# Optimization experiments

Hardware: AMD Instinct MI355X
Metric: run time of the kernel (lower is better)

The kernel has to match this reference:

```python
import jax, jax.numpy as jnp
import numpy as np

ALG = 8  # octonion algebra dimension
_TRIPLES = [(1,2,3),(1,4,5),(1,7,6),(2,4,6),(2,5,7),(3,4,7),(3,6,5)]

def _oct_table():
    # Cayley multiplication table: e_i * e_j = S[i,j] * e_{K[i,j]}
    K = np.zeros((8,8), np.int64); S = np.zeros((8,8), np.int64)
    K[0,:] = np.arange(8); S[0,:] = 1
    K[:,0] = np.arange(8); S[:,0] = 1
    for i in range(1,8):
        K[i,i] = 0; S[i,i] = -1
    for (a,b,c) in _TRIPLES:
        for x,y,z in ((a,b,c),(b,c,a),(c,a,b)):
            K[x,y] = z; S[x,y] = 1
            K[y,x] = z; S[y,x] = -1
    return K, S

_K, _S = _oct_table()

def _ternary(w):
    # BitNet-style absmean ternary quantization (STE is irrelevant for fwd)
    scale = jnp.mean(jnp.abs(w)) + 1e-8
    wq = jnp.clip(jnp.round(w / scale), -1.0, 1.0) * scale
    return w + jax.lax.stop_gradient(wq - w)

def _oct_big(w):
    # w: [8, din8, dout8] -> structured dense [8*din8, 8*dout8]
    # out_k = sum_{i,j: e_i e_j = s e_k} s * x_i @ W_j  (64 static blocks)
    din8, dout8 = w.shape[1], w.shape[2]
    big = jnp.zeros((8, din8, 8, dout8), w.dtype)
    for i in range(8):
        for j in range(8):
            big = big.at[i, :, int(_K[i, j]), :].set(float(_S[i, j]) * w[j])
    return big.reshape(8 * din8, 8 * dout8)

def _oct_linear(x, w):
    return x @ _oct_big(_ternary(w))

def setup_inputs() -> dict:
    key = jax.random.key(0)
    k1, k2, k3, k4 = jax.random.split(key, 4)
    B, T, D = 8, 4096, 768
    H = 2048  # int(2*4*768/3) rounded up to multiple of 8
    d8, h8 = D // ALG, H // ALG
    x = jax.random.normal(k1, (B, T, D), dtype=jnp.float32)
    w_gate = 0.02 * jax.random.normal(k2, (ALG, d8, h8), dtype=jnp.float32)
    w_up   = 0.02 * jax.random.normal(k3, (ALG, d8, h8), dtype=jnp.float32)
    w_down = 0.02 * jax.random.normal(k4, (ALG, h8, d8), dtype=jnp.float32)
    return {"x": x, "w_gate": w_gate, "w_up": w_up, "w_down": w_down}

def reference(x, w_gate, w_up, w_down):
    gate = _oct_linear(x, w_gate)          # [B,T,H]
    up   = _oct_linear(x, w_up)            # [B,T,H]
    h    = jax.nn.silu(gate) * up          # SwiGLU gate
    return _oct_linear(h, w_down)          # [B,T,D]
```

## Files before the change

### kernel.cpp

```cpp
#include <hip/hip_runtime.h>
#include <hip/hip_bf16.h>

typedef unsigned short u16;
typedef unsigned int u32;
typedef float f32x4 __attribute__((ext_vector_type(4)));
typedef __bf16 bf16x8 __attribute__((ext_vector_type(8)));

#define AS1 __attribute__((address_space(1)))
#define AS3 __attribute__((address_space(3)))

#define MTOT 32768
#define DK   768
#define HN   2048

__constant__ signed char J_TAB[64] = {
  0,1,2,3,4,5,6,7,
  1,0,3,2,5,4,7,6,
  2,3,0,1,6,7,4,5,
  3,2,1,0,7,6,5,4,
  4,5,6,7,0,1,2,3,
  5,4,7,6,1,0,3,2,
  6,7,4,5,2,3,0,1,
  7,6,5,4,3,2,1,0};
__constant__ signed char S_TAB[64] = {
   1, 1, 1, 1, 1, 1, 1, 1,
  -1, 1,-1, 1,-1, 1, 1,-1,
  -1, 1, 1,-1,-1,-1, 1, 1,
  -1,-1, 1, 1,-1, 1,-1, 1,
  -1, 1, 1, 1, 1,-1,-1,-1,
  -1,-1, 1,-1, 1, 1, 1,-1,
  -1,-1,-1, 1, 1,-1, 1, 1,
  -1, 1,-1,-1, 1, 1,-1, 1};

__device__ __forceinline__ u16 f2bf(float f) {
  u32 x = __float_as_uint(f);
  x += 0x7fffu + ((x >> 16) & 1u);
  return (u16)(x >> 16);
}

__device__ __forceinline__ void gload_lds16(const void* g, void* l) {
  __builtin_amdgcn_global_load_lds((AS1 void*)(g), (AS3 void*)(l), 16, 0, 0);
}

template <int ROWS>
__device__ __forceinline__ void stage_tile(const u16* __restrict__ src, int ldk,
                                           u16* lds, int tid) {
#pragma unroll
  for (int f0 = 0; f0 < ROWS * 8; f0 += 256) {
    int flat = f0 + tid;
    int row = flat >> 3;
    int c = (flat & 7) ^ (row & 7);
    gload_lds16(src + row * ldk + c * 8, lds + (f0 + (tid & 192)) * 8);
  }
}

__device__ __forceinline__ bf16x8 frag64(const u16* lds, int row, int cbase) {
  int c = cbase ^ (row & 7);
  return *(const bf16x8*)(lds + row * 64 + c * 8);
}

__global__ void scales1_kernel(const float* __restrict__ w0,
                               const float* __restrict__ w1,
                               const float* __restrict__ w2,
                               float* __restrict__ partials) {
  __shared__ float red[256];
  const int t = blockIdx.x / 192;
  const int chunk = blockIdx.x % 192;
  const float* w = (t == 0) ? w0 : (t == 1) ? w1 : w2;
  const float4* w4 = (const float4*)(w + chunk * 1024);
  float4 v = w4[threadIdx.x];
  red[threadIdx.x] = fabsf(v.x) + fabsf(v.y) + fabsf(v.z) + fabsf(v.w);
  __syncthreads();
  for (int off = 128; off; off >>= 1) {
    if (threadIdx.x < off) red[threadIdx.x] += red[threadIdx.x + off];
    __syncthreads();
  }
  if (threadIdx.x == 0) partials[blockIdx.x] = red[0];
}

__global__ void scales2_kernel(const float* __restrict__ partials,
                               float* __restrict__ scales) {
  __shared__ float red[256];
  float s = (threadIdx.x < 192) ? partials[blockIdx.x * 192 + threadIdx.x] : 0.f;
  red[threadIdx.x] = s;
  __syncthreads();
  for (int off = 128; off; off >>= 1) {
    if (threadIdx.x < off) red[threadIdx.x] += red[threadIdx.x + off];
    __syncthreads();
  }
  if (threadIdx.x == 0) scales[blockIdx.x] = red[0] / 196608.f + 1e-8f;
}

__global__ void build_big_kernel(const float* __restrict__ w,
                                 const float* __restrict__ scales, int sidx,
                                 int A, int B, u16* __restrict__ dst) {
  int idx = blockIdx.x * 256 + threadIdx.x;
  int K8 = 8 * A;
  int n = idx / K8;
  int k = idx - n * K8;
  int i = k / A, a = k - i * A;
  int c = n / B, b = n - c * B;
  float scale = scales[sidx];
  int j = J_TAB[i * 8 + c];
  float q = rintf(w[(j * A + a) * B + b] / scale);
  q = fminf(1.f, fmaxf(-1.f, q));
  dst[idx] = f2bf(q * (float)S_TAB[i * 8 + c]);
}

__global__ void cvt_x_kernel(const float* __restrict__ x, u16* __restrict__ xb) {
  int gid = blockIdx.x * 256 + threadIdx.x;
  const float4* x4 = (const float4*)x;
  float4 v0 = x4[gid * 2], v1 = x4[gid * 2 + 1];
  uint4 o;
  o.x = (u32)f2bf(v0.x) | ((u32)f2bf(v0.y) << 16);
  o.y = (u32)f2bf(v0.z) | ((u32)f2bf(v0.w) << 16);
  o.z = (u32)f2bf(v1.x) | ((u32)f2bf(v1.y) << 16);
  o.w = (u32)f2bf(v1.z) | ((u32)f2bf(v1.w) << 16);
  ((uint4*)xb)[gid] = o;
}

__global__ __launch_bounds__(256) void gemm1_kernel(
    const u16* __restrict__ xb, const u16* __restrict__ wg,
    const u16* __restrict__ wu, const float* __restrict__ scales,
    u16* __restrict__ h) {
  __shared__ __align__(16) u16 lA[128 * 64];
  __shared__ __align__(16) u16 lG[64 * 64];
  __shared__ __align__(16) u16 lU[64 * 64];
  const int tid = threadIdx.x;
  const int bn = blockIdx.x & 31;
  const int bm = blockIdx.x >> 5;
  const int m0 = bm * 128, n0 = bn * 64;
  const int lane = tid & 63, wave = tid >> 6;
  const int wm = wave >> 1, wn = wave & 1;
  const int l15 = lane & 15, quad = lane >> 4;

  f32x4 accG[4][2] = {};
  f32x4 accU[4][2] = {};

  const u16* aSrc = xb + m0 * DK;
  const u16* gSrc = wg + n0 * DK;
  const u16* uSrc = wu + n0 * DK;

  for (int k0 = 0; k0 < DK; k0 += 64) {
    stage_tile<128>(aSrc + k0, DK, lA, tid);
    stage_tile<64>(gSrc + k0, DK, lG, tid);
    stage_tile<64>(uSrc + k0, DK, lU, tid);
    __syncthreads();
#pragma unroll
    for (int ks = 0; ks < 2; ++ks) {
      const int cb = ks * 4 + quad;
      bf16x8 af[4], gf[2], uf[2];
#pragma unroll
      for (int mi = 0; mi < 4; ++mi)
        af[mi] = frag64(lA, wm * 64 + mi * 16 + l15, cb);
#pragma unroll
      for (int ni = 0; ni < 2; ++ni) {
        gf[ni] = frag64(lG, wn * 32 + ni * 16 + l15, cb);
        uf[ni] = frag64(lU, wn * 32 + ni * 16 + l15, cb);
      }
#pragma unroll
      for (int mi = 0; mi < 4; ++mi)
#pragma unroll
        for (int ni = 0; ni < 2; ++ni) {
          accG[mi][ni] = __builtin_amdgcn_mfma_f32_16x16x32_bf16(
              af[mi], gf[ni], accG[mi][ni], 0, 0, 0);
          accU[mi][ni] = __builtin_amdgcn_mfma_f32_16x16x32_bf16(
              af[mi], uf[ni], accU[mi][ni], 0, 0, 0);
        }
    }
    __syncthreads();
  }

  const float sg = scales[0], su = scales[1];
#pragma unroll
  for (int mi = 0; mi < 4; ++mi)
#pragma unroll
    for (int ni = 0; ni < 2; ++ni)
#pragma unroll
      for (int r = 0; r < 4; ++r) {
        int m = m0 + wm * 64 + mi * 16 + quad * 4 + r;
        int n = n0 + wn * 32 + ni * 16 + l15;
        float g = accG[mi][ni][r] * sg;
        float u = accU[mi][ni][r] * su;
        float hv = g / (1.f + __expf(-g)) * u;
        h[m * HN + n] = f2bf(hv);
      }
}

__global__ __launch_bounds__(256) void gemm2_kernel(
    const u16* __restrict__ h, const u16* __restrict__ wd,
    const float* __restrict__ scales, float* __restrict__ out) {
  __shared__ __align__(16) u16 lA[128 * 64];
  __shared__ __align__(16) u16 lB[128 * 64];
  const int tid = threadIdx.x;
  const int bn = blockIdx.x % 6;
  const int bm = blockIdx.x / 6;
  const int m0 = bm * 128, n0 = bn * 128;
  const int lane = tid & 63, wave = tid >> 6;
  const int wm = wave >> 1, wn = wave & 1;
  const int l15 = lane & 15, quad = lane >> 4;

  f32x4 acc[4][4] = {};

  const u16* aSrc = h + m0 * HN;
  const u16* bSrc = wd + n0 * HN;

  for (int k0 = 0; k0 < HN; k0 += 64) {
    stage_tile<128>(aSrc + k0, HN, lA, tid);
    stage_tile<128>(bSrc + k0, HN, lB, tid);
    __syncthreads();
#pragma unroll
    for (int ks = 0; ks < 2; ++ks) {
      const int cb = ks * 4 + quad;
      bf16x8 af[4], bf[4];
#pragma unroll
      for (int mi = 0; mi < 4; ++mi)
        af[mi] = frag64(lA, wm * 64 + mi * 16 + l15, cb);
#pragma unroll
      for (int ni = 0; ni < 4; ++ni)
        bf[ni] = frag64(lB, wn * 64 + ni * 16 + l15, cb);
#pragma unroll
      for (int mi = 0; mi < 4; ++mi)
#pragma unroll
        for (int ni = 0; ni < 4; ++ni)
          acc[mi][ni] = __builtin_amdgcn_mfma_f32_16x16x32_bf16(
              af[mi], bf[ni], acc[mi][ni], 0, 0, 0);
    }
    __syncthreads();
  }

  const float sd = scales[2];
#pragma unroll
  for (int mi = 0; mi < 4; ++mi)
#pragma unroll
    for (int ni = 0; ni < 4; ++ni)
#pragma unroll
      for (int r = 0; r < 4; ++r) {
        int m = m0 + wm * 64 + mi * 16 + quad * 4 + r;
        int n = n0 + wn * 64 + ni * 16 + l15;
        out[m * DK + n] = acc[mi][ni][r] * sd;
      }
}

extern "C" void kernel_launch(void* const* d_in, const int* in_sizes, int n_in,
                              void* d_out, int out_size, void* d_ws, size_t ws_size,
                              hipStream_t stream) {
  const float* x      = (const float*)d_in[0];
  const float* w_gate = (const float*)d_in[1];
  const float* w_up   = (const float*)d_in[2];
  const float* w_down = (const float*)d_in[3];
  float* out = (float*)d_out;

  char* ws = (char*)d_ws;
  float* scales   = (float*)ws;
  float* partials = (float*)(ws + 256);
  u16* wg = (u16*)(ws + 4096);
  u16* wu = (u16*)(ws + 4096 + 1u * 3145728u);
  u16* wd = (u16*)(ws + 4096 + 2u * 3145728u);
  u16* xb = (u16*)(ws + 4096 + 3u * 3145728u);
  u16* h  = (u16*)(ws + 4096 + 3u * 3145728u + 50331648u);

  scales1_kernel<<<576, 256, 0, stream>>>(w_gate, w_up, w_down, partials);
  scales2_kernel<<<3, 256, 0, stream>>>(partials, scales);
  build_big_kernel<<<6144, 256, 0, stream>>>(w_gate, scales, 0, 96, 256, wg);
  build_big_kernel<<<6144, 256, 0, stream>>>(w_up,   scales, 1, 96, 256, wu);
  build_big_kernel<<<6144, 256, 0, stream>>>(w_down, scales, 2, 256, 96, wd);
  cvt_x_kernel<<<12288, 256, 0, stream>>>(x, xb);
  gemm1_kernel<<<8192, 256, 0, stream>>>(xb, wg, wu, scales, h);
  gemm2_kernel<<<1536, 256, 0, stream>>>(h, wd, scales, out);
}
```

Baseline: 597.1 us.

## Pre-swizzle weights into MFMA fragment layout and load B operands directly from global

The weight-building kernel now writes the ternary weight matrices in an MFMA-fragment-ordered layout (16 rows by 32 k per 64-lane line), so each lane can fetch its B fragment with one 16-byte global load. Both GEMMs drop the LDS staging for weights and read B fragments straight from global/L2, which cuts LDS traffic and shared-memory use. gemm1 also widens its N tile from 64 to 128, doubling accumulators and halving the grid. The trade-off is more global-load latency exposed inside the k-loop with no prefetching, plus higher register pressure in gemm1.

```diff
diff --git a/kernel.cpp b/kernel.cpp
--- a/kernel.cpp
+++ b/kernel.cpp
@@ -93,18 +93,28 @@
 
 __global__ void build_big_kernel(const float* __restrict__ w,
                                  const float* __restrict__ scales, int sidx,
-                                 int A, int B, u16* __restrict__ dst) {
-  int idx = blockIdx.x * 256 + threadIdx.x;
-  int K8 = 8 * A;
-  int n = idx / K8;
-  int k = idx - n * K8;
-  int i = k / A, a = k - i * A;
+                                 int A, int B, int KT, u16* __restrict__ dst) {
+  int L = blockIdx.x * 256 + threadIdx.x;
+  int lane = L & 63;
+  int ntkt = L >> 6;
+  int kt = ntkt % KT;
+  int nt = ntkt / KT;
+  int n = nt * 16 + (lane & 15);
+  int kb = kt * 32 + (lane >> 4) * 8;
   int c = n / B, b = n - c * B;
+  int i = kb / A, a0 = kb - i * A;
   float scale = scales[sidx];
+  float s = (float)S_TAB[i * 8 + c];
   int j = J_TAB[i * 8 + c];
-  float q = rintf(w[(j * A + a) * B + b] / scale);
-  q = fminf(1.f, fmaxf(-1.f, q));
-  dst[idx] = f2bf(q * (float)S_TAB[i * 8 + c]);
+  const float* src = w + (j * A + a0) * B + b;
+  u16 vals[8];
+#pragma unroll
+  for (int jj = 0; jj < 8; ++jj) {
+    float q = rintf(src[jj * B] / scale);
+    q = fminf(1.f, fmaxf(-1.f, q));
+    vals[jj] = f2bf(q * s);
+  }
+  *(uint4*)(dst + L * 8) = *(uint4*)vals;
 }
 
 __global__ void cvt_x_kernel(const float* __restrict__ x, u16* __restrict__ xb) {
@@ -120,48 +130,50 @@
 }
 
 __global__ __launch_bounds__(256) void gemm1_kernel(
-    const u16* __restrict__ xb, const u16* __restrict__ wg,
-    const u16* __restrict__ wu, const float* __restrict__ scales,
+    const u16* __restrict__ xb, const u16* __restrict__ wgf,
+    const u16* __restrict__ wuf, const float* __restrict__ scales,
     u16* __restrict__ h) {
   __shared__ __align__(16) u16 lA[128 * 64];
-  __shared__ __align__(16) u16 lG[64 * 64];
-  __shared__ __align__(16) u16 lU[64 * 64];
   const int tid = threadIdx.x;
-  const int bn = blockIdx.x & 31;
-  const int bm = blockIdx.x >> 5;
-  const int m0 = bm * 128, n0 = bn * 64;
+  const int bn = blockIdx.x & 15;
+  const int bm = blockIdx.x >> 4;
+  const int m0 = bm * 128, n0 = bn * 128;
   const int lane = tid & 63, wave = tid >> 6;
   const int wm = wave >> 1, wn = wave & 1;
   const int l15 = lane & 15, quad = lane >> 4;
-
-  f32x4 accG[4][2] = {};
-  f32x4 accU[4][2] = {};
+  const int KT1 = DK / 32;
+
+  f32x4 accG[4][4] = {};
+  f32x4 accU[4][4] = {};
 
   const u16* aSrc = xb + m0 * DK;
-  const u16* gSrc = wg + n0 * DK;
-  const u16* uSrc = wu + n0 * DK;
+  const bf16x8* gLines = (const bf16x8*)wgf;
+  const bf16x8* uLines = (const bf16x8*)wuf;
+  const int ntBase = (n0 + wn * 64) >> 4;
 
   for (int k0 = 0; k0 < DK; k0 += 64) {
     stage_tile<128>(aSrc + k0, DK, lA, tid);
-    stage_tile<64>(gSrc + k0, DK, lG, tid);
-    stage_tile<64>(uSrc + k0, DK, lU, tid);
-    __syncthreads();
+    __syncthreads();
+    const int ktBase = k0 >> 5;
 #pragma unroll
     for (int ks = 0; ks < 2; ++ks) {
+      const int kt = ktBase + ks;
+      bf16x8 gf[4], uf[4];
+#pragma unroll
+      for (int ni = 0; ni < 4; ++ni) {
+        const int line = ((ntBase + ni) * KT1 + kt) * 64 + lane;
+        gf[ni] = gLines[line];
+        uf[ni] = uLines[line];
+      }
       const int cb = ks * 4 + quad;
-      bf16x8 af[4], gf[2], uf[2];
+      bf16x8 af[4];
 #pragma unroll
       for (int mi = 0; mi < 4; ++mi)
         af[mi] = frag64(lA, wm * 64 + mi * 16 + l15, cb);
 #pragma unroll
-      for (int ni = 0; ni < 2; ++ni) {
-        gf[ni] = frag64(lG, wn * 32 + ni * 16 + l15, cb);
-        uf[ni] = frag64(lU, wn * 32 + ni * 16 + l15, cb);
-      }
-#pragma unroll
-      for (int mi = 0; mi < 4; ++mi)
-#pragma unroll
-        for (int ni = 0; ni < 2; ++ni) {
+      for (int mi = 0; mi < 4; ++mi)
+#pragma unroll
+        for (int ni = 0; ni < 4; ++ni) {
           accG[mi][ni] = __builtin_amdgcn_mfma_f32_16x16x32_bf16(
               af[mi], gf[ni], accG[mi][ni], 0, 0, 0);
           accU[mi][ni] = __builtin_amdgcn_mfma_f32_16x16x32_bf16(
@@ -175,11 +187,11 @@
 #pragma unroll
   for (int mi = 0; mi < 4; ++mi)
 #pragma unroll
-    for (int ni = 0; ni < 2; ++ni)
+    for (int ni = 0; ni < 4; ++ni)
 #pragma unroll
       for (int r = 0; r < 4; ++r) {
         int m = m0 + wm * 64 + mi * 16 + quad * 4 + r;
-        int n = n0 + wn * 32 + ni * 16 + l15;
+        int n = n0 + wn * 64 + ni * 16 + l15;
         float g = accG[mi][ni][r] * sg;
         float u = accU[mi][ni][r] * su;
         float hv = g / (1.f + __expf(-g)) * u;
@@ -188,10 +200,9 @@
 }
 
 __global__ __launch_bounds__(256) void gemm2_kernel(
-    const u16* __restrict__ h, const u16* __restrict__ wd,
+    const u16* __restrict__ h, const u16* __restrict__ wdf,
     const float* __restrict__ scales, float* __restrict__ out) {
   __shared__ __align__(16) u16 lA[128 * 64];
-  __shared__ __align__(16) u16 lB[128 * 64];
   const int tid = threadIdx.x;
   const int bn = blockIdx.x % 6;
   const int bm = blockIdx.x / 6;
@@ -199,32 +210,36 @@
   const int lane = tid & 63, wave = tid >> 6;
   const int wm = wave >> 1, wn = wave & 1;
   const int l15 = lane & 15, quad = lane >> 4;
+  const int KT2 = HN / 32;
 
   f32x4 acc[4][4] = {};
 
   const u16* aSrc = h + m0 * HN;
-  const u16* bSrc = wd + n0 * HN;
+  const bf16x8* dLines = (const bf16x8*)wdf;
+  const int ntBase = (n0 + wn * 64) >> 4;
 
   for (int k0 = 0; k0 < HN; k0 += 64) {
     stage_tile<128>(aSrc + k0, HN, lA, tid);
-    stage_tile<128>(bSrc + k0, HN, lB, tid);
-    __syncthreads();
+    __syncthreads();
+    const int ktBase = k0 >> 5;
 #pragma unroll
     for (int ks = 0; ks < 2; ++ks) {
+      const int kt = ktBase + ks;
+      bf16x8 bfr[4];
+#pragma unroll
+      for (int ni = 0; ni < 4; ++ni)
+        bfr[ni] = dLines[((ntBase + ni) * KT2 + kt) * 64 + lane];
       const int cb = ks * 4 + quad;
-      bf16x8 af[4], bf[4];
+      bf16x8 af[4];
 #pragma unroll
       for (int mi = 0; mi < 4; ++mi)
         af[mi] = frag64(lA, wm * 64 + mi * 16 + l15, cb);
-#pragma unroll
-      for (int ni = 0; ni < 4; ++ni)
-        bf[ni] = frag64(lB, wn * 64 + ni * 16 + l15, cb);
 #pragma unroll
       for (int mi = 0; mi < 4; ++mi)
 #pragma unroll
         for (int ni = 0; ni < 4; ++ni)
           acc[mi][ni] = __builtin_amdgcn_mfma_f32_16x16x32_bf16(
-              af[mi], bf[ni], acc[mi][ni], 0, 0, 0);
+              af[mi], bfr[ni], acc[mi][ni], 0, 0, 0);
     }
     __syncthreads();
   }
@@ -262,10 +277,10 @@
 
   scales1_kernel<<<576, 256, 0, stream>>>(w_gate, w_up, w_down, partials);
   scales2_kernel<<<3, 256, 0, stream>>>(partials, scales);
-  build_big_kernel<<<6144, 256, 0, stream>>>(w_gate, scales, 0, 96, 256, wg);
-  build_big_kernel<<<6144, 256, 0, stream>>>(w_up,   scales, 1, 96, 256, wu);
-  build_big_kernel<<<6144, 256, 0, stream>>>(w_down, scales, 2, 256, 96, wd);
+  build_big_kernel<<<768, 256, 0, stream>>>(w_gate, scales, 0, 96, 256, DK / 32, wg);
+  build_big_kernel<<<768, 256, 0, stream>>>(w_up,   scales, 1, 96, 256, DK / 32, wu);
+  build_big_kernel<<<768, 256, 0, stream>>>(w_down, scales, 2, 256, 96, HN / 32, wd);
   cvt_x_kernel<<<12288, 256, 0, stream>>>(x, xb);
-  gemm1_kernel<<<8192, 256, 0, stream>>>(xb, wg, wu, scales, h);
+  gemm1_kernel<<<4096, 256, 0, stream>>>(xb, wg, wu, scales, h);
   gemm2_kernel<<<1536, 256, 0, stream>>>(h, wd, scales, out);
 }
```

Measured after the change: 845.6 us. 1.42x slower.

## Enlarge GEMM tiles and transpose MFMA operands for vectorized epilogue stores

Applied to the files above, without the earlier changes.

The gemm1 N-tile grows from 64 to 128 and the gemm2 M-tile from 128 to 256, so each block reuses more staged data per load and fewer blocks are launched. The MFMA operand order is swapped so each lane holds four consecutive output columns. That lets the epilogue write packed 64-bit bf16 and 128-bit float stores instead of scalar ones. The cost is more registers and LDS per block (gemm2 holds 128 accumulator floats per lane), which lowers occupancy and could cause register spills.

```diff
diff --git a/kernel.cpp b/kernel.cpp
--- a/kernel.cpp
+++ b/kernel.cpp
@@ -124,18 +124,18 @@
     const u16* __restrict__ wu, const float* __restrict__ scales,
     u16* __restrict__ h) {
   __shared__ __align__(16) u16 lA[128 * 64];
-  __shared__ __align__(16) u16 lG[64 * 64];
-  __shared__ __align__(16) u16 lU[64 * 64];
+  __shared__ __align__(16) u16 lG[128 * 64];
+  __shared__ __align__(16) u16 lU[128 * 64];
   const int tid = threadIdx.x;
-  const int bn = blockIdx.x & 31;
-  const int bm = blockIdx.x >> 5;
-  const int m0 = bm * 128, n0 = bn * 64;
+  const int bn = blockIdx.x & 15;
+  const int bm = blockIdx.x >> 4;
+  const int m0 = bm * 128, n0 = bn * 128;
   const int lane = tid & 63, wave = tid >> 6;
   const int wm = wave >> 1, wn = wave & 1;
   const int l15 = lane & 15, quad = lane >> 4;
 
-  f32x4 accG[4][2] = {};
-  f32x4 accU[4][2] = {};
+  f32x4 accG[4][4] = {};
+  f32x4 accU[4][4] = {};
 
   const u16* aSrc = xb + m0 * DK;
   const u16* gSrc = wg + n0 * DK;
@@ -143,29 +143,29 @@
 
   for (int k0 = 0; k0 < DK; k0 += 64) {
     stage_tile<128>(aSrc + k0, DK, lA, tid);
-    stage_tile<64>(gSrc + k0, DK, lG, tid);
-    stage_tile<64>(uSrc + k0, DK, lU, tid);
+    stage_tile<128>(gSrc + k0, DK, lG, tid);
+    stage_tile<128>(uSrc + k0, DK, lU, tid);
     __syncthreads();
 #pragma unroll
     for (int ks = 0; ks < 2; ++ks) {
       const int cb = ks * 4 + quad;
-      bf16x8 af[4], gf[2], uf[2];
+      bf16x8 af[4], gf[4], uf[4];
 #pragma unroll
       for (int mi = 0; mi < 4; ++mi)
         af[mi] = frag64(lA, wm * 64 + mi * 16 + l15, cb);
 #pragma unroll
-      for (int ni = 0; ni < 2; ++ni) {
-        gf[ni] = frag64(lG, wn * 32 + ni * 16 + l15, cb);
-        uf[ni] = frag64(lU, wn * 32 + ni * 16 + l15, cb);
+      for (int ni = 0; ni < 4; ++ni) {
+        gf[ni] = frag64(lG, wn * 64 + ni * 16 + l15, cb);
+        uf[ni] = frag64(lU, wn * 64 + ni * 16 + l15, cb);
       }
 #pragma unroll
       for (int mi = 0; mi < 4; ++mi)
 #pragma unroll
-        for (int ni = 0; ni < 2; ++ni) {
+        for (int ni = 0; ni < 4; ++ni) {
           accG[mi][ni] = __builtin_amdgcn_mfma_f32_16x16x32_bf16(
-              af[mi], gf[ni], accG[mi][ni], 0, 0, 0);
+              gf[ni], af[mi], accG[mi][ni], 0, 0, 0);
           accU[mi][ni] = __builtin_amdgcn_mfma_f32_16x16x32_bf16(
-              af[mi], uf[ni], accU[mi][ni], 0, 0, 0);
+              uf[ni], af[mi], accU[mi][ni], 0, 0, 0);
         }
     }
     __syncthreads();
@@ -173,73 +173,77 @@
 
   const float sg = scales[0], su = scales[1];
 #pragma unroll
-  for (int mi = 0; mi < 4; ++mi)
-#pragma unroll
-    for (int ni = 0; ni < 2; ++ni)
+  for (int mi = 0; mi < 4; ++mi) {
+    const int m = m0 + wm * 64 + mi * 16 + l15;
+    u16* hrow = h + m * HN + n0 + wn * 64 + quad * 4;
+#pragma unroll
+    for (int ni = 0; ni < 4; ++ni) {
+      u16 vals[4];
 #pragma unroll
       for (int r = 0; r < 4; ++r) {
-        int m = m0 + wm * 64 + mi * 16 + quad * 4 + r;
-        int n = n0 + wn * 32 + ni * 16 + l15;
         float g = accG[mi][ni][r] * sg;
         float u = accU[mi][ni][r] * su;
         float hv = g / (1.f + __expf(-g)) * u;
-        h[m * HN + n] = f2bf(hv);
+        vals[r] = f2bf(hv);
       }
+      *(uint2*)(hrow + ni * 16) = *(uint2*)vals;
+    }
+  }
 }
 
 __global__ __launch_bounds__(256) void gemm2_kernel(
     const u16* __restrict__ h, const u16* __restrict__ wd,
     const float* __restrict__ scales, float* __restrict__ out) {
-  __shared__ __align__(16) u16 lA[128 * 64];
+  __shared__ __align__(16) u16 lA[256 * 64];
   __shared__ __align__(16) u16 lB[128 * 64];
   const int tid = threadIdx.x;
   const int bn = blockIdx.x % 6;
   const int bm = blockIdx.x / 6;
-  const int m0 = bm * 128, n0 = bn * 128;
+  const int m0 = bm * 256, n0 = bn * 128;
   const int lane = tid & 63, wave = tid >> 6;
   const int wm = wave >> 1, wn = wave & 1;
   const int l15 = lane & 15, quad = lane >> 4;
 
-  f32x4 acc[4][4] = {};
+  f32x4 acc[8][4] = {};
 
   const u16* aSrc = h + m0 * HN;
   const u16* bSrc = wd + n0 * HN;
 
   for (int k0 = 0; k0 < HN; k0 += 64) {
-    stage_tile<128>(aSrc + k0, HN, lA, tid);
+    stage_tile<256>(aSrc + k0, HN, lA, tid);
     stage_tile<128>(bSrc + k0, HN, lB, tid);
     __syncthreads();
 #pragma unroll
     for (int ks = 0; ks < 2; ++ks) {
       const int cb = ks * 4 + quad;
-      bf16x8 af[4], bf[4];
-#pragma unroll
-      for (int mi = 0; mi < 4; ++mi)
-        af[mi] = frag64(lA, wm * 64 + mi * 16 + l15, cb);
+      bf16x8 af[8], bfr[4];
+#pragma unroll
+      for (int mi = 0; mi < 8; ++mi)
+        af[mi] = frag64(lA, wm * 128 + mi * 16 + l15, cb);
 #pragma unroll
       for (int ni = 0; ni < 4; ++ni)
-        bf[ni] = frag64(lB, wn * 64 + ni * 16 + l15, cb);
-#pragma unroll
-      for (int mi = 0; mi < 4; ++mi)
+        bfr[ni] = frag64(lB, wn * 64 + ni * 16 + l15, cb);
+#pragma unroll
+      for (int mi = 0; mi < 8; ++mi)
 #pragma unroll
         for (int ni = 0; ni < 4; ++ni)
           acc[mi][ni] = __builtin_amdgcn_mfma_f32_16x16x32_bf16(
-              af[mi], bf[ni], acc[mi][ni], 0, 0, 0);
+              bfr[ni], af[mi], acc[mi][ni], 0, 0, 0);
     }
     __syncthreads();
   }
 
   const float sd = scales[2];
 #pragma unroll
-  for (int mi = 0; mi < 4; ++mi)
-#pragma unroll
-    for (int ni = 0; ni < 4; ++ni)
-#pragma unroll
-      for (int r = 0; r < 4; ++r) {
-        int m = m0 + wm * 64 + mi * 16 + quad * 4 + r;
-        int n = n0 + wn * 64 + ni * 16 + l15;
-        out[m * DK + n] = acc[mi][ni][r] * sd;
-      }
+  for (int mi = 0; mi < 8; ++mi) {
+    const int m = m0 + wm * 128 + mi * 16 + l15;
+    float* orow = out + m * DK + n0 + wn * 64 + quad * 4;
+#pragma unroll
+    for (int ni = 0; ni < 4; ++ni) {
+      f32x4 v = acc[mi][ni] * sd;
+      *(f32x4*)(orow + ni * 16) = v;
+    }
+  }
 }
 
 extern "C" void kernel_launch(void* const* d_in, const int* in_sizes, int n_in,
@@ -266,6 +270,6 @@
   build_big_kernel<<<6144, 256, 0, stream>>>(w_up,   scales, 1, 96, 256, wu);
   build_big_kernel<<<6144, 256, 0, stream>>>(w_down, scales, 2, 256, 96, wd);
   cvt_x_kernel<<<12288, 256, 0, stream>>>(x, xb);
-  gemm1_kernel<<<8192, 256, 0, stream>>>(xb, wg, wu, scales, h);
-  gemm2_kernel<<<1536, 256, 0, stream>>>(h, wd, scales, out);
-}
+  gemm1_kernel<<<4096, 256, 0, stream>>>(xb, wg, wu, scales, h);
+  gemm2_kernel<<<768, 256, 0, stream>>>(h, wd, scales, out);
+}
```

After: 788.6 us. +32.1%, slower.
